# Kernel tuning notes

Measured on AMD Instinct MI355X. Metric: run time of the kernel, lower is better.

Reference implementation:

```python
import jax, jax.numpy as jnp
import numpy as np

SCALE, K, PATCH, STRIDE = 2, 5, 3, 1
EPS = 1e-5


def im2patch(x, p, s):
    # x: (b,c,H,W) -> (b,c,p,p,m1,m2), 'VALID' patches (padding is 0 for our sizes)
    b, c, H, W = x.shape
    m1 = (H - p) // s + 1
    m2 = (W - p) // s + 1
    ii = (jnp.arange(m1) * s)[:, None] + jnp.arange(p)[None, :]   # (m1,p)
    jj = (jnp.arange(m2) * s)[:, None] + jnp.arange(p)[None, :]   # (m2,p)
    pt = x[:, :, ii[:, :, None, None], jj[None, None, :, :]]      # (b,c,m1,p,m2,p)
    return pt.transpose(0, 1, 3, 5, 2, 4)                         # (b,c,p,p,m1,m2)


def patch2im(patches, p, s):
    # overlap-add fold, averaged by per-pixel patch counts (torch F.fold / ones-fold divisor)
    b, c, _, _, m1, m2 = patches.shape
    Hp = (m1 - 1) * s + p
    Wp = (m2 - 1) * s + p
    out = jnp.zeros((b, c, Hp, Wp), patches.dtype)
    cnt = jnp.zeros((Hp, Wp), patches.dtype)
    for i in range(p):          # fixed small loop over patch offsets (p*p = 36)
        for j in range(p):
            out = out.at[:, :, i:i + s * m1:s, j:j + s * m2:s].add(patches[:, :, i, j])
            cnt = cnt.at[i:i + s * m1:s, j:j + s * m2:s].add(1.0)
    return out / cnt


def setup_inputs():
    key = jax.random.key(0)
    k1, k2, k3 = jax.random.split(key, 3)
    b, cy, H, W = 1, 64, 80, 80
    y = jax.random.normal(k1, (b, cy, H, W), jnp.float32)
    yd = jax.random.normal(k2, (b, cy * SCALE ** 2, H // SCALE, W // SCALE), jnp.float32)
    m = ((H - PATCH) // STRIDE + 1) ** 2
    n = ((H // SCALE - PATCH) // STRIDE + 1) ** 2
    idx_k = jax.random.randint(k3, (b, m, K), 0, n, jnp.int32)
    return {"y": y, "yd": yd, "idx_k": idx_k}


def reference(y, yd, idx_k):
    b, cy, H, W = y.shape
    c = yd.shape[1]           # = cy * scale^2
    rs = SCALE ** 2
    y_p = im2patch(y, PATCH, STRIDE)      # (b,cy,p,p,m1,m2)
    yd_p = im2patch(yd, PATCH, STRIDE)    # (b,c,p,p,n1,n2)
    m1, m2 = y_p.shape[-2:]
    n1, n2 = yd_p.shape[-2:]
    m, n = m1 * m2, n1 * n2
    f = c * PATCH * PATCH
    y_flat = y_p.transpose(0, 4, 5, 1, 2, 3).reshape(b, m, f // rs)
    yd_flat = yd_p.transpose(0, 4, 5, 1, 2, 3).reshape(b, n, f)
    # top-k neighbor gather: (b,n,f)[idx (b,m,k)] -> (b,m,k,f) -> (b,m,f,k)
    z = jax.vmap(lambda t, i: t[i])(yd_flat, idx_k)
    z = z.transpose(0, 1, 3, 2)
    # AdaIN: normalize gathered HR patches, apply LR query patch stats (unbiased var, torch default)
    y_n = y_flat.reshape(b, m, c // rs, PATCH * PATCH)
    z_n = z.reshape(b, m, c // rs, rs * PATCH * PATCH, K)
    z_mu = z_n.mean(axis=3, keepdims=True)
    z_sd = jnp.sqrt(z_n.var(axis=3, ddof=1, keepdims=True) + EPS)
    y_mu = y_n.mean(axis=3, keepdims=True)[..., None]        # (b,m,c',1,1)
    y_sd = jnp.sqrt(y_n.var(axis=3, ddof=1, keepdims=True) + EPS)[..., None]
    z = ((z_n - z_mu) / z_sd * y_sd + y_mu).reshape(b, m, f, K)
    # rearrange f = (cy, scale, scale, p1, p2) into SR patches (b, k*cy, p*scale, p*scale, m1, m2)
    z = z.transpose(0, 3, 2, 1)                                   # (b,k,f,m)
    z = z.reshape(b, K, cy, SCALE, SCALE, PATCH, PATCH, m1, m2)
    z = z.transpose(0, 1, 2, 5, 3, 6, 4, 7, 8)                    # (b,k,cy,p1,s,p2,s,m1,m2)
    z = z.reshape(b, K * cy, PATCH * SCALE, PATCH * SCALE, m1, m2)
    z_sr = patch2im(z, PATCH * SCALE, STRIDE * SCALE)             # (b,k*cy,H*scale,W*scale)
    return z_sr.reshape(b, K * cy, H * SCALE, W * SCALE)
```

## Files before the change

### kernel.cpp

```cpp
#include <hip/hip_runtime.h>
#include <hip/hip_fp16.h>
#include <string.h>

#define CY     64
#define HY     80
#define HD     40
#define SPD    (HD*HD)
#define M1     78
#define N1     38
#define M_TOT  (M1*M1)
#define N_TOT  (N1*N1)
#define KK     5
#define HS     160
#define EPSF   1e-5f
#define LP     33

typedef float f32x2 __attribute__((ext_vector_type(2)));

__device__ __forceinline__ unsigned pkf16(float a, float b) {
    __half2 h = __floats2half2_rn(a, b);
    unsigned u; memcpy(&u, &h, 4); return u;
}
__device__ __forceinline__ f32x2 upk2(unsigned u) {
    __half2 h; memcpy(&h, &u, 4);
    float2 f = __half22float2(h);
    f32x2 r; r.x = f.x; r.y = f.y; return r;
}

__global__ __launch_bounds__(256) void stats_kernel(const float* __restrict__ y,
                                                    const float* __restrict__ yd,
                                                    unsigned* __restrict__ zstP,
                                                    unsigned* __restrict__ ystP) {
    int id = blockIdx.x * 256 + threadIdx.x;
    if (id < N_TOT * 64) {
        int n  = id % N_TOT;
        int cc = id / N_TOT;
        int ni = n / N1, nj = n - ni * N1;
        const float* base = yd + (cc * 4) * SPD + ni * HD + nj;
        float s = 0.f, sq = 0.f;
#pragma unroll
        for (int r = 0; r < 4; ++r)
#pragma unroll
            for (int i = 0; i < 3; ++i)
#pragma unroll
                for (int j = 0; j < 3; ++j) {
                    float v = base[r * SPD + i * HD + j];
                    s += v; sq += v * v;
                }
        float mu  = s * (1.f / 36.f);
        float var = (sq - 36.f * mu * mu) * (1.f / 35.f);
        zstP[n * 64 + cc] = pkf16(mu, rsqrtf(var + EPSF));
        return;
    }
    id -= N_TOT * 64;
    if (id >= CY * M_TOT) return;
    int m  = id % M_TOT;
    int cc = id / M_TOT;
    int mi = m / M1, mj = m - mi * M1;
    const float* base = y + cc * (HY * HY) + mi * HY + mj;
    float s = 0.f, sq = 0.f;
#pragma unroll
    for (int i = 0; i < 3; ++i)
#pragma unroll
        for (int j = 0; j < 3; ++j) {
            float v = base[i * HY + j];
            s += v; sq += v * v;
        }
    float mu  = s * (1.f / 9.f);
    float var = (sq - 9.f * mu * mu) * (1.f / 8.f);
    ystP[m * 64 + cc] = pkf16(mu, sqrtf(var + EPSF));
}

__global__ __launch_bounds__(256) void coef_kernel(const float* __restrict__ yd,
        const int* __restrict__ idx, const unsigned* __restrict__ zstP,
        const unsigned* __restrict__ ystP, unsigned* __restrict__ coefP,
        int* __restrict__ nsp, uint4* __restrict__ ydW) {
    int gid = blockIdx.x * 256 + threadIdx.x;
    if (gid < KK * M_TOT * 64) {
        int cc   = gid & 63;
        int pair = gid >> 6;
        int k = pair / M_TOT, m = pair - k * M_TOT;
        int n = idx[m * KK + k];
        f32x2 ys = upk2(ystP[m * 64 + cc]);
        f32x2 zs = upk2(zstP[n * 64 + cc]);
        float a = ys.y * zs.y;
        float b = fmaf(-zs.x, a, ys.x);
        coefP[(size_t)pair * 64 + cc] = pkf16(a, b);
        if (cc == 0) { int ni = n / N1; nsp[pair] = ni * HD + (n - ni * N1); }
        return;
    }
    gid -= KK * M_TOT * 64;
    int sp = gid % SPD, cc = gid / SPD;
    const float* b0 = yd + (cc * 4) * SPD + sp;
    int d = (sp < SPD - 1) ? 1 : 0;
    float a0 = b0[0],       a1 = b0[SPD],     a2 = b0[2*SPD],   a3 = b0[3*SPD];
    float c0 = b0[d],       c1 = b0[SPD+d],   c2 = b0[2*SPD+d], c3 = b0[3*SPD+d];
    ydW[sp * 64 + cc] = make_uint4(pkf16(a0, a1), pkf16(a2, a3),
                                   pkf16(c0, c1), pkf16(c2, c3));
}

__global__ __launch_bounds__(512) void agg_kernel(
    const uint4* __restrict__ ydW, const unsigned* __restrict__ coefP,
    const int* __restrict__ nsp, float* __restrict__ out)
{
    __shared__ float lds[128 * LP];

    int lane = threadIdx.x & 63;
    int w    = __builtin_amdgcn_readfirstlane(threadIdx.x >> 6);
    int bid  = blockIdx.x;
    int wg   = (bid & 7) * 250 + (bid >> 3);
    int k    = wg / 400;
    int rem  = wg - k * 400;
    int y    = rem / 5;
    int xb2  = rem - y * 5;
    int x0   = xb2 * 16 + w * 2;

    const unsigned* cfk  = coefP + (size_t)k * M_TOT * 64;
    const int*      nspk = nsp + k * M_TOT;

    f32x2 acc01[2] = {{0.f,0.f},{0.f,0.f}};
    f32x2 acc23[2] = {{0.f,0.f},{0.f,0.f}};
    float bs[2] = {0.f, 0.f};
    float inv0, inv1;

    auto serve = [&](f32x2& a01, f32x2& a23, float& bsum,
                     unsigned lo, unsigned hi, float a, float b) {
        f32x2 am; am.x = a; am.y = a;
        a01 = __builtin_elementwise_fma(am, upk2(lo), a01);
        a23 = __builtin_elementwise_fma(am, upk2(hi), a23);
        bsum += b;
    };

    if (y >= 2 && y <= M1 - 1 && x0 >= 2 && x0 <= M1 - 2) {
        inv0 = inv1 = 1.f / 9.f;
        unsigned cfu[12];
        int spb[12];
#pragma unroll
        for (int p = 0; p < 12; ++p) {
            int m = (y - 2 + (p >> 2)) * M1 + (x0 - 2 + (p & 3));
            cfu[p] = cfk[m * 64 + lane];
            spb[p] = nspk[m];
        }
        float aa[12], bb[12];
#pragma unroll
        for (int p = 0; p < 12; ++p) {
            f32x2 c = upk2(cfu[p]);
            aa[p] = c.x; bb[p] = c.y;
        }
#pragma unroll
        for (int r = 0; r < 3; ++r) {
            int roff = (2 - r) * HD;
            int s0 = spb[r*4+0] + roff, s1 = spb[r*4+1] + roff;
            int s2 = spb[r*4+2] + roff, s3 = spb[r*4+3] + roff;
            uint2 v0 = *(const uint2*)(ydW + (s0 + 2) * 64 + lane);
            uint4 v1 = ydW[(s1 + 1) * 64 + lane];
            uint4 v2 = ydW[(s2 + 0) * 64 + lane];
            uint2 v3 = *(const uint2*)(ydW + (s3 + 0) * 64 + lane);
            serve(acc01[0], acc23[0], bs[0], v0.x, v0.y, aa[r*4+0], bb[r*4+0]);
            serve(acc01[0], acc23[0], bs[0], v1.x, v1.y, aa[r*4+1], bb[r*4+1]);
            serve(acc01[1], acc23[1], bs[1], v1.z, v1.w, aa[r*4+1], bb[r*4+1]);
            serve(acc01[0], acc23[0], bs[0], v2.x, v2.y, aa[r*4+2], bb[r*4+2]);
            serve(acc01[1], acc23[1], bs[1], v2.z, v2.w, aa[r*4+2], bb[r*4+2]);
            serve(acc01[1], acc23[1], bs[1], v3.x, v3.y, aa[r*4+3], bb[r*4+3]);
        }
    } else {
#pragma unroll
        for (int q = 0; q < 2; ++q) {
            int x = x0 + q;
            int milo = max(0, y - 2), mihi = min(M1 - 1, y);
            int mjlo = max(0, x - 2), mjhi = min(M1 - 1, x);
            float iv = 1.f / (float)((mihi - milo + 1) * (mjhi - mjlo + 1));
            if (q == 0) inv0 = iv; else inv1 = iv;
            for (int mi = milo; mi <= mihi; ++mi)
                for (int mj = mjlo; mj <= mjhi; ++mj) {
                    int m = mi * M1 + mj;
                    f32x2 c = upk2(cfk[m * 64 + lane]);
                    int sp = nspk[m] + (y - mi) * HD + (x - mj);
                    uint2 v = *(const uint2*)(ydW + sp * 64 + lane);
                    if (q == 0) serve(acc01[0], acc23[0], bs[0], v.x, v.y, c.x, c.y);
                    else        serve(acc01[1], acc23[1], bs[1], v.x, v.y, c.x, c.y);
                }
        }
    }

#pragma unroll
    for (int q = 0; q < 2; ++q) {
        float iv = q ? inv1 : inv0;
        float bq = bs[q];
        int col = (w * 2 + q) * 2;
        lds[(0 * CY + lane) * LP + col]     = (acc01[q].x + bq) * iv;
        lds[(0 * CY + lane) * LP + col + 1] = (acc01[q].y + bq) * iv;
        lds[(1 * CY + lane) * LP + col]     = (acc23[q].x + bq) * iv;
        lds[(1 * CY + lane) * LP + col + 1] = (acc23[q].y + bq) * iv;
    }

    __syncthreads();

    int rsel = lane >> 5, c = lane & 31;
    int X0 = xb2 * 32, Y0 = 2 * y;
#pragma unroll
    for (int t = 0; t < 8; ++t) {
        int row = t * 16 + w * 2 + rsel;
        float v = lds[row * LP + c];
        int dy = row >> 6, cc = row & 63;
        out[((size_t)(k * CY + cc) * HS + (Y0 + dy)) * HS + X0 + c] = v;
    }
}

extern "C" void kernel_launch(void* const* d_in, const int* in_sizes, int n_in,
                              void* d_out, int out_size, void* d_ws, size_t ws_size,
                              hipStream_t stream) {
    const float* y   = (const float*)d_in[0];
    const float* yd  = (const float*)d_in[1];
    const int*   idx = (const int*)d_in[2];
    float* out = (float*)d_out;

    char* ws = (char*)d_ws;
    uint4*    ydW   = (uint4*)ws;
    unsigned* zstP  = (unsigned*)(ws + 1638400);
    unsigned* ystP  = (unsigned*)(ws + 2008064);
    unsigned* coefP = (unsigned*)(ws + 3565568);
    int*      nspb  = (int*)(ws + 11353088);

    int stats_total = N_TOT * 64 + CY * M_TOT;
    stats_kernel<<<(stats_total + 255) / 256, 256, 0, stream>>>(y, yd, zstP, ystP);
    int coef_total = KK * M_TOT * 64 + SPD * 64;
    coef_kernel<<<(coef_total + 255) / 256, 256, 0, stream>>>(yd, idx, zstP, ystP,
                                                              coefP, nspb, ydW);
    agg_kernel<<<KK * 400, 512, 0, stream>>>(ydW, coefP, nspb, out);
}
```

Measured before the change: 38.35 us.

## Fuse coefficient computation into aggregation kernel and drop coef pass

```diff
diff --git a/kernel.cpp b/kernel.cpp
--- a/kernel.cpp
+++ b/kernel.cpp
@@ -27,11 +27,23 @@
     f32x2 r; r.x = f.x; r.y = f.y; return r;
 }
 
-__global__ __launch_bounds__(256) void stats_kernel(const float* __restrict__ y,
-                                                    const float* __restrict__ yd,
-                                                    unsigned* __restrict__ zstP,
-                                                    unsigned* __restrict__ ystP) {
+__global__ __launch_bounds__(256) void pre_kernel(const float* __restrict__ y,
+                                                  const float* __restrict__ yd,
+                                                  uint4* __restrict__ ydW,
+                                                  unsigned* __restrict__ zstP,
+                                                  unsigned* __restrict__ ystP) {
     int id = blockIdx.x * 256 + threadIdx.x;
+    if (id < SPD * 64) {
+        int cc = id & 63, sp = id >> 6;
+        const float* b0 = yd + (cc * 4) * SPD + sp;
+        int d = (sp < SPD - 1) ? 1 : 0;
+        ydW[sp * 64 + cc] = make_uint4(pkf16(b0[0], b0[SPD]),
+                                       pkf16(b0[2*SPD], b0[3*SPD]),
+                                       pkf16(b0[d], b0[SPD+d]),
+                                       pkf16(b0[2*SPD+d], b0[3*SPD+d]));
+        return;
+    }
+    id -= SPD * 64;
     if (id < N_TOT * 64) {
         int n  = id % N_TOT;
         int cc = id / N_TOT;
@@ -71,37 +83,10 @@
     ystP[m * 64 + cc] = pkf16(mu, sqrtf(var + EPSF));
 }
 
-__global__ __launch_bounds__(256) void coef_kernel(const float* __restrict__ yd,
-        const int* __restrict__ idx, const unsigned* __restrict__ zstP,
-        const unsigned* __restrict__ ystP, unsigned* __restrict__ coefP,
-        int* __restrict__ nsp, uint4* __restrict__ ydW) {
-    int gid = blockIdx.x * 256 + threadIdx.x;
-    if (gid < KK * M_TOT * 64) {
-        int cc   = gid & 63;
-        int pair = gid >> 6;
-        int k = pair / M_TOT, m = pair - k * M_TOT;
-        int n = idx[m * KK + k];
-        f32x2 ys = upk2(ystP[m * 64 + cc]);
-        f32x2 zs = upk2(zstP[n * 64 + cc]);
-        float a = ys.y * zs.y;
-        float b = fmaf(-zs.x, a, ys.x);
-        coefP[(size_t)pair * 64 + cc] = pkf16(a, b);
-        if (cc == 0) { int ni = n / N1; nsp[pair] = ni * HD + (n - ni * N1); }
-        return;
-    }
-    gid -= KK * M_TOT * 64;
-    int sp = gid % SPD, cc = gid / SPD;
-    const float* b0 = yd + (cc * 4) * SPD + sp;
-    int d = (sp < SPD - 1) ? 1 : 0;
-    float a0 = b0[0],       a1 = b0[SPD],     a2 = b0[2*SPD],   a3 = b0[3*SPD];
-    float c0 = b0[d],       c1 = b0[SPD+d],   c2 = b0[2*SPD+d], c3 = b0[3*SPD+d];
-    ydW[sp * 64 + cc] = make_uint4(pkf16(a0, a1), pkf16(a2, a3),
-                                   pkf16(c0, c1), pkf16(c2, c3));
-}
-
 __global__ __launch_bounds__(512) void agg_kernel(
-    const uint4* __restrict__ ydW, const unsigned* __restrict__ coefP,
-    const int* __restrict__ nsp, float* __restrict__ out)
+    const uint4* __restrict__ ydW, const unsigned* __restrict__ zstP,
+    const unsigned* __restrict__ ystP, const int* __restrict__ idx,
+    float* __restrict__ out)
 {
     __shared__ float lds[128 * LP];
 
@@ -115,9 +100,6 @@
     int xb2  = rem - y * 5;
     int x0   = xb2 * 16 + w * 2;
 
-    const unsigned* cfk  = coefP + (size_t)k * M_TOT * 64;
-    const int*      nspk = nsp + k * M_TOT;
-
     f32x2 acc01[2] = {{0.f,0.f},{0.f,0.f}};
     f32x2 acc23[2] = {{0.f,0.f},{0.f,0.f}};
     float bs[2] = {0.f, 0.f};
@@ -133,19 +115,26 @@
 
     if (y >= 2 && y <= M1 - 1 && x0 >= 2 && x0 <= M1 - 2) {
         inv0 = inv1 = 1.f / 9.f;
-        unsigned cfu[12];
-        int spb[12];
+        unsigned ysu[12], zsu[12];
+        int nn[12];
 #pragma unroll
         for (int p = 0; p < 12; ++p) {
             int m = (y - 2 + (p >> 2)) * M1 + (x0 - 2 + (p & 3));
-            cfu[p] = cfk[m * 64 + lane];
-            spb[p] = nspk[m];
-        }
+            nn[p]  = idx[m * KK + k];
+            ysu[p] = ystP[m * 64 + lane];
+        }
+#pragma unroll
+        for (int p = 0; p < 12; ++p)
+            zsu[p] = zstP[nn[p] * 64 + lane];
         float aa[12], bb[12];
+        int spb[12];
 #pragma unroll
         for (int p = 0; p < 12; ++p) {
-            f32x2 c = upk2(cfu[p]);
-            aa[p] = c.x; bb[p] = c.y;
+            f32x2 ys = upk2(ysu[p]), zs = upk2(zsu[p]);
+            aa[p] = ys.y * zs.y;
+            bb[p] = fmaf(-zs.x, aa[p], ys.x);
+            int n = nn[p], ni = n / N1;
+            spb[p] = ni * HD + (n - ni * N1);
         }
 #pragma unroll
         for (int r = 0; r < 3; ++r) {
@@ -174,11 +163,16 @@
             for (int mi = milo; mi <= mihi; ++mi)
                 for (int mj = mjlo; mj <= mjhi; ++mj) {
                     int m = mi * M1 + mj;
-                    f32x2 c = upk2(cfk[m * 64 + lane]);
-                    int sp = nspk[m] + (y - mi) * HD + (x - mj);
+                    int n = idx[m * KK + k];
+                    f32x2 ys = upk2(ystP[m * 64 + lane]);
+                    f32x2 zs = upk2(zstP[n * 64 + lane]);
+                    float a = ys.y * zs.y;
+                    float b = fmaf(-zs.x, a, ys.x);
+                    int ni = n / N1;
+                    int sp = ni * HD + (n - ni * N1) + (y - mi) * HD + (x - mj);
                     uint2 v = *(const uint2*)(ydW + sp * 64 + lane);
-                    if (q == 0) serve(acc01[0], acc23[0], bs[0], v.x, v.y, c.x, c.y);
-                    else        serve(acc01[1], acc23[1], bs[1], v.x, v.y, c.x, c.y);
+                    if (q == 0) serve(acc01[0], acc23[0], bs[0], v.x, v.y, a, b);
+                    else        serve(acc01[1], acc23[1], bs[1], v.x, v.y, a, b);
                 }
         }
     }
@@ -216,16 +210,11 @@
     float* out = (float*)d_out;
 
     char* ws = (char*)d_ws;
-    uint4*    ydW   = (uint4*)ws;
-    unsigned* zstP  = (unsigned*)(ws + 1638400);
-    unsigned* ystP  = (unsigned*)(ws + 2008064);
-    unsigned* coefP = (unsigned*)(ws + 3565568);
-    int*      nspb  = (int*)(ws + 11353088);
-
-    int stats_total = N_TOT * 64 + CY * M_TOT;
-    stats_kernel<<<(stats_total + 255) / 256, 256, 0, stream>>>(y, yd, zstP, ystP);
-    int coef_total = KK * M_TOT * 64 + SPD * 64;
-    coef_kernel<<<(coef_total + 255) / 256, 256, 0, stream>>>(yd, idx, zstP, ystP,
-                                                              coefP, nspb, ydW);
-    agg_kernel<<<KK * 400, 512, 0, stream>>>(ydW, coefP, nspb, out);
-}
+    uint4*    ydW  = (uint4*)ws;
+    unsigned* zstP = (unsigned*)(ws + 1638400);
+    unsigned* ystP = (unsigned*)(ws + 2008064);
+
+    int pre_total = SPD * 64 + N_TOT * 64 + CY * M_TOT;
+    pre_kernel<<<(pre_total + 255) / 256, 256, 0, stream>>>(y, yd, ydW, zstP, ystP);
+    agg_kernel<<<KK * 400, 512, 0, stream>>>(ydW, zstP, ystP, idx, out);
+}
```

After: 35.47 us. 7.5% less time.
